# Kernel optimization log

Measured on AMD Instinct MI355X. Metric: run time of the kernel, lower is better.

The kernel has to match this reference:

```python
import jax, jax.numpy as jnp
import numpy as np

N_HEAD = 16
MA_K = 0.02          # sigmoid temperature in ma_k_activation
LEAKY_SLOPE = 0.02   # negative_slope in ma_q_activation
NEG_INF = -1e9


def setup_inputs() -> dict:
    key = jax.random.key(0)
    k1, k2, k3, k4 = jax.random.split(key, 4)
    B, T, C = 2, 2048, 1024
    x = jax.random.normal(k1, (B, T, C), dtype=jnp.float32)
    s = 1.0 / np.sqrt(C)
    W_attn = jax.random.normal(k2, (C, 2 * C), dtype=jnp.float32) * s
    W_k2 = jax.random.normal(k3, (C, C), dtype=jnp.float32) * s
    W_proj = jax.random.normal(k4, (C, C), dtype=jnp.float32) * s
    return {"x": x, "W_attn": W_attn, "W_k2": W_k2, "W_proj": W_proj}


def _heads(t, H):
    # [B,T,C] -> [B,H,T,d]
    B, T, C = t.shape
    return t.reshape(B, T, H, C // H).transpose(0, 2, 1, 3)


def reference(x, W_attn, W_k2, W_proj):
    B, T, C = x.shape
    H = N_HEAD
    d = C // H
    scale = 1.0 / jnp.sqrt(jnp.asarray(d, x.dtype))

    qk = x @ W_attn                      # [B,T,2C]
    q, k = jnp.split(qk, 2, axis=-1)
    q = _heads(q, H)                     # [B,H,T,d]
    k = _heads(k, H)
    v = _heads(x, H)                     # v = x

    # --- AR branch: causal softmax attention ---
    scores = jnp.einsum('bhtd,bhsd->bhts', q, k) * scale
    causal = jnp.tril(jnp.ones((T, T), dtype=bool))
    scores = jnp.where(causal, scores, NEG_INF)
    attn = jax.nn.softmax(scores, axis=-1)
    y = jnp.einsum('bhts,bhsd->bhtd', attn, v)   # [B,H,T,d]

    # --- MA branch: causal, softmax-free linear attention on residual ---
    e = v[:, :, 1:, :] - y[:, :, :-1, :]          # [B,H,T-1,d]
    k2 = _heads(x[:, :-1, :] @ W_k2, H)           # [B,H,T-1,d]
    q2 = q[:, :, 1:, :]                           # [B,H,T-1,d]

    qa = -jax.nn.leaky_relu(-q2 * scale, negative_slope=LEAKY_SLOPE)
    ka = jax.nn.sigmoid(MA_K * (k2 * scale))

    w = jnp.einsum('bhtd,bhsd->bhts', qa, ka)     # [B,H,T-1,T-1]
    w = jnp.tril(w)
    y2 = jnp.einsum('bhts,bhsd->bhtd', w, e)      # [B,H,T-1,d]
    y2 = jnp.concatenate([jnp.zeros_like(y2[:, :, :1, :]), y2], axis=2)  # pad front

    def merge(t):  # [B,H,T,d] -> [B,T,C]
        return t.transpose(0, 2, 1, 3).reshape(B, T, C)

    return merge(y) @ W_proj + merge(y2) @ W_proj
```

## Files before the change

kernel.cpp:

```cpp
#include <hip/hip_runtime.h>

typedef unsigned short u16;
typedef u16   u16x4  __attribute__((ext_vector_type(4)));
typedef u16   u16x8  __attribute__((ext_vector_type(8)));
typedef __bf16 bf16x8 __attribute__((ext_vector_type(8)));
typedef float  f32x4  __attribute__((ext_vector_type(4)));

__device__ __forceinline__ float bf2f(u16 v) {
    unsigned u = ((unsigned)v) << 16;
    return __builtin_bit_cast(float, u);
}
__device__ __forceinline__ u16 f2bf(float f) {
    unsigned u = __builtin_bit_cast(unsigned, f);
    u += 0x7fffu + ((u >> 16) & 1u);
    return (u16)(u >> 16);
}

__device__ __forceinline__ void async16(const u16* g, u16* l) {
    __builtin_amdgcn_global_load_lds(
        (const __attribute__((address_space(1))) unsigned int*)g,
        (__attribute__((address_space(3))) unsigned int*)l,
        16, 0, 0);
}

__device__ __forceinline__ size_t kimg_idx(int bh, int s, int d) {
    return ((size_t)(bh * 32 + (s >> 6)) * 4096) + (size_t)(((d >> 3) * 64 + (s & 63)) * 8) + (d & 7);
}
__device__ __forceinline__ size_t vimg_idx(int bh, int s, int d) {
    return ((size_t)(bh * 32 + (s >> 6)) * 4096) + (size_t)((((s & 63) >> 3) * 64 + d) * 8) + (s & 7);
}

__device__ __forceinline__ size_t g128_idx(int m, int k) {
    return ((size_t)((m >> 7) * 32 + (k >> 5)) * 4096)
         + (size_t)((((k >> 3) & 3) * 128 + (m & 127)) * 8 + (k & 7));
}
__device__ __forceinline__ size_t g64_idx(int m, int k) {
    return ((size_t)((m >> 6) * 32 + (k >> 5)) * 2048)
         + (size_t)((((k >> 3) & 3) * 64 + (m & 63)) * 8 + (k & 7));
}

__global__ __launch_bounds__(256)
void convert_pack(const float* __restrict__ in, u16* __restrict__ xb,
                  u16* __restrict__ xpack, u16* __restrict__ agimg) {
    int i = blockIdx.x * 256 + threadIdx.x;
    int c8 = i & 127, row = i >> 7;
    int s = row & 2047, b = row >> 11;
    float4 v0 = ((const float4*)in)[(size_t)i * 2];
    float4 v1 = ((const float4*)in)[(size_t)i * 2 + 1];
    u16x8 o;
    o[0] = f2bf(v0.x); o[1] = f2bf(v0.y); o[2] = f2bf(v0.z); o[3] = f2bf(v0.w);
    o[4] = f2bf(v1.x); o[5] = f2bf(v1.y); o[6] = f2bf(v1.z); o[7] = f2bf(v1.w);
    ((u16x8*)xb)[i] = o;
    int h = c8 >> 3, d0 = (c8 & 7) * 8;
    size_t base = vimg_idx(b * 16 + h, s, d0);
#pragma unroll
    for (int j = 0; j < 8; ++j) xpack[base + j * 8] = o[j];
    *(u16x8*)&agimg[g128_idx(row, c8 * 8)] = o;
}

__global__ __launch_bounds__(256)
void prep_weights(const float* __restrict__ Wa, const float* __restrict__ Wk,
                  const float* __restrict__ Wp, u16* __restrict__ bgimg,
                  u16* __restrict__ bpimg) {
    __shared__ u16 tile[64][65];
    const int bx = blockIdx.x;
    const float* in; u16* img; int Cd, c0, nbase;
    if (bx < 32)      { in = Wa; img = bgimg; Cd = 2048; c0 = bx * 64;        nbase = c0; }
    else if (bx < 48) { in = Wk; img = bgimg; Cd = 1024; c0 = (bx - 32) * 64; nbase = 2048 + c0; }
    else              { in = Wp; img = bpimg; Cd = 1024; c0 = (bx - 48) * 64; nbase = c0; }
    const int r0 = blockIdx.y * 64;
    const int tid = threadIdx.x;
#pragma unroll
    for (int i = 0; i < 16; ++i) {
        int idx = tid + i * 256;
        int r = idx >> 6, c = idx & 63;
        tile[r][c] = f2bf(in[(size_t)(r0 + r) * Cd + c0 + c]);
    }
    __syncthreads();
#pragma unroll
    for (int ii = 0; ii < 16; ++ii) {
        int u = tid + ii * 256;
        int s = u >> 11, kk = (u >> 9) & 3, nr = (u >> 3) & 63, e = u & 7;
        int r = s * 32 + kk * 8 + e;
        int n = nbase + nr, k = r0 + r;
        size_t o = (size_t)((n >> 7) * 32 + (k >> 5)) * 4096
                 + (size_t)(kk * 1024 + (n & 127) * 8 + e);
        img[o] = tile[r][nr];
    }
}

__global__ __launch_bounds__(256, 3)
void gemm_fused(const u16* __restrict__ Aimg, const u16* __restrict__ Bimg,
                u16* __restrict__ qs, u16* __restrict__ kpack,
                u16* __restrict__ kapack) {
    const int NT = 32;
    __shared__ __align__(16) u16 As[3][4][128][8];
    __shared__ __align__(16) u16 Bs[3][4][128][8];
    const int tid = threadIdx.x;
    const int wave = tid >> 6, lane = tid & 63;
    const int m0 = blockIdx.y * 128, n0 = blockIdx.x * 128;
    const int wm = (wave >> 1) * 64, wn = (wave & 1) * 64;
    const int q = lane >> 4, mr = lane & 15;

    const u16* gA = Aimg + (size_t)blockIdx.y * 32 * 4096;
    const u16* gB = Bimg + (size_t)blockIdx.x * 32 * 4096;
    u16* const lA = &As[0][0][0][0];
    u16* const lB = &Bs[0][0][0][0];
    const int d0 = tid * 8, d1 = (256 + tid) * 8;

    f32x4 acc[4][4];
#pragma unroll
    for (int i = 0; i < 4; ++i)
#pragma unroll
        for (int j = 0; j < 4; ++j) acc[i][j] = f32x4{0.f, 0.f, 0.f, 0.f};

    async16(gA + d0,        lA + d0);
    async16(gA + d1,        lA + d1);
    async16(gB + d0,        lB + d0);
    async16(gB + d1,        lB + d1);
    async16(gA + 4096 + d0, lA + 4096 + d0);
    async16(gA + 4096 + d1, lA + 4096 + d1);
    async16(gB + 4096 + d0, lB + 4096 + d0);
    async16(gB + 4096 + d1, lB + 4096 + d1);

    int co = 0;
    int io = 2 * 4096;
    for (int t = 0; t < NT; ++t) {
        if (t < NT - 1) asm volatile("s_waitcnt vmcnt(4)" ::: "memory");
        else            asm volatile("s_waitcnt vmcnt(0)" ::: "memory");
        __syncthreads();
        if (t + 2 < NT) {
            const int sg = (t + 2) * 4096;
            async16(gA + sg + d0, lA + io + d0);
            async16(gA + sg + d1, lA + io + d1);
            async16(gB + sg + d0, lB + io + d0);
            async16(gB + sg + d1, lB + io + d1);
        }
        bf16x8 af[4], bfr[4];
#pragma unroll
        for (int i = 0; i < 4; ++i)
            af[i]  = *(const bf16x8*)(lA + co + (size_t)(q * 128 + wm + i * 16 + mr) * 8);
#pragma unroll
        for (int j = 0; j < 4; ++j)
            bfr[j] = *(const bf16x8*)(lB + co + (size_t)(q * 128 + wn + j * 16 + mr) * 8);
#pragma unroll
        for (int i = 0; i < 4; ++i)
#pragma unroll
            for (int j = 0; j < 4; ++j)
                acc[i][j] = __builtin_amdgcn_mfma_f32_16x16x32_bf16(af[i], bfr[j], acc[i][j], 0, 0, 0);
        co += 4096; if (co == 3 * 4096) co = 0;
        io += 4096; if (io == 3 * 4096) io = 0;
    }
#pragma unroll
    for (int i = 0; i < 4; ++i)
#pragma unroll
        for (int j = 0; j < 4; ++j)
#pragma unroll
            for (int r = 0; r < 4; ++r) {
                int m = m0 + wm + i * 16 + q * 4 + r;
                int n = n0 + wn + j * 16 + mr;
                float v = acc[i][j][r];
                int b = m >> 11, s = m & 2047;
                if (n < 1024) {
                    qs[(size_t)m * 1024 + n] = f2bf(v * 0.125f);
                } else if (n < 2048) {
                    int nn = n - 1024;
                    kpack[kimg_idx(b * 16 + (nn >> 6), s, nn & 63)] = f2bf(v);
                } else {
                    int nn = n - 2048;
                    kapack[kimg_idx(b * 16 + (nn >> 6), s, nn & 63)] =
                        f2bf(1.f / (1.f + __expf(-0.0025f * v)));
                }
            }
}

__global__ __launch_bounds__(256, 2)
void gemm64(const u16* __restrict__ Aimg, const u16* __restrict__ Bimg,
            float* __restrict__ Cv, int N, int K) {
    const int NT = 32;
    __shared__ __align__(16) u16 As[3][4][64][8];
    __shared__ __align__(16) u16 Bs[3][4][128][8];
    const int tid = threadIdx.x;
    const int wave = tid >> 6, lane = tid & 63;
    const int m0 = blockIdx.y * 64, n0 = blockIdx.x * 128;
    const int wn0 = wave * 32;
    const int q = lane >> 4, mr = lane & 15;

    const u16* gA = Aimg + (size_t)blockIdx.y * 32 * 2048;
    const u16* gB = Bimg + (size_t)blockIdx.x * 32 * 4096;
    u16* const lA = &As[0][0][0][0];
    u16* const lB = &Bs[0][0][0][0];
    const int d0 = tid * 8, d1 = (256 + tid) * 8;

    f32x4 acc[4][2];
#pragma unroll
    for (int i = 0; i < 4; ++i)
#pragma unroll
        for (int j = 0; j < 2; ++j) acc[i][j] = f32x4{0.f, 0.f, 0.f, 0.f};

    async16(gA + d0,        lA + d0);
    async16(gB + d0,        lB + d0);
    async16(gB + d1,        lB + d1);
    async16(gA + 2048 + d0, lA + 2048 + d0);
    async16(gB + 4096 + d0, lB + 4096 + d0);
    async16(gB + 4096 + d1, lB + 4096 + d1);

    int coA = 0, coB = 0, ioA = 2 * 2048, ioB = 2 * 4096;
    for (int t = 0; t < NT; ++t) {
        if (t < NT - 1) asm volatile("s_waitcnt vmcnt(3)" ::: "memory");
        else            asm volatile("s_waitcnt vmcnt(0)" ::: "memory");
        __syncthreads();
        if (t + 2 < NT) {
            async16(gA + (t + 2) * 2048 + d0, lA + ioA + d0);
            async16(gB + (t + 2) * 4096 + d0, lB + ioB + d0);
            async16(gB + (t + 2) * 4096 + d1, lB + ioB + d1);
        }
        bf16x8 af[4], bfr[2];
#pragma unroll
        for (int i = 0; i < 4; ++i)
            af[i]  = *(const bf16x8*)(lA + coA + (size_t)(q * 64 + i * 16 + mr) * 8);
#pragma unroll
        for (int j = 0; j < 2; ++j)
            bfr[j] = *(const bf16x8*)(lB + coB + (size_t)(q * 128 + wn0 + j * 16 + mr) * 8);
#pragma unroll
        for (int i = 0; i < 4; ++i)
#pragma unroll
            for (int j = 0; j < 2; ++j)
                acc[i][j] = __builtin_amdgcn_mfma_f32_16x16x32_bf16(af[i], bfr[j], acc[i][j], 0, 0, 0);
        coA += 2048; if (coA == 3 * 2048) coA = 0;
        coB += 4096; if (coB == 3 * 4096) coB = 0;
        ioA += 2048; if (ioA == 3 * 2048) ioA = 0;
        ioB += 4096; if (ioB == 3 * 4096) ioB = 0;
    }
#pragma unroll
    for (int i = 0; i < 4; ++i)
#pragma unroll
        for (int j = 0; j < 2; ++j)
#pragma unroll
            for (int r = 0; r < 4; ++r) {
                int m = m0 + i * 16 + q * 4 + r;
                int n = n0 + wn0 + j * 16 + mr;
                Cv[(size_t)m * N + n] = acc[i][j][r];
            }
}

__global__ __launch_bounds__(256, 2)
void flash_mfma(const u16* __restrict__ qs, const u16* __restrict__ kpack,
                const u16* __restrict__ xpack, u16* __restrict__ Opart,
                float* __restrict__ lpart) {
    __shared__ __align__(16) u16 Ks[8][64][8];
    __shared__ __align__(16) u16 Vs[8][64][8];
    __shared__ __align__(16) u16 Ps[4][16][72];
    const int bh = blockIdx.y, b = bh >> 4, hc = (bh & 15) * 64;
    const int z = blockIdx.z;
    const int tid = threadIdx.x, w = tid >> 6, lane = tid & 63;
    const int n16 = lane & 15, quad = lane >> 4;
    const u16* kbase = kpack + (size_t)bh * 32 * 4096;
    const u16* vbase = xpack + (size_t)bh * 32 * 4096;
    u16* Ob = Opart + (size_t)z * 4096 * 1024;
    float* lb = lpart + z * 65536;

    for (int rep = 0; rep < 2; ++rep) {
        const int T = rep ? 15 - (int)blockIdx.x : (int)blockIdx.x;
        const int t0 = T * 128;
        const int nchunk = 2 * T + 2;

        bf16x8 qf[2][2];
#pragma unroll
        for (int mt = 0; mt < 2; ++mt) {
            const int trow = t0 + (w + mt * 4) * 16 + n16;
            const u16* qp = &qs[(size_t)(b * 2048 + trow) * 1024 + hc + quad * 8];
            qf[mt][0] = *(const bf16x8*)qp;
            qf[mt][1] = *(const bf16x8*)(qp + 32);
        }

        f32x4 O[2][4];
        float lsum[2][4];
#pragma unroll
        for (int mt = 0; mt < 2; ++mt)
#pragma unroll
            for (int jt = 0; jt < 4; ++jt) { O[mt][jt] = f32x4{0.f, 0.f, 0.f, 0.f}; }
#pragma unroll
        for (int mt = 0; mt < 2; ++mt)
#pragma unroll
            for (int r = 0; r < 4; ++r) lsum[mt][r] = 0.f;

        u16x8 kr0, kr1, vr0, vr1;
        auto pref = [&](int c) {
            const u16* kc = kbase + (size_t)c * 4096;
            const u16* vc = vbase + (size_t)c * 4096;
            kr0 = *(const u16x8*)(kc + tid * 8);
            kr1 = *(const u16x8*)(kc + (256 + tid) * 8);
            vr0 = *(const u16x8*)(vc + tid * 8);
            vr1 = *(const u16x8*)(vc + (256 + tid) * 8);
        };
        if (z < nchunk) pref(z);

        for (int c = z; c < nchunk; c += 2) {
            __syncthreads();
            *(u16x8*)((u16*)Ks + tid * 8)         = kr0;
            *(u16x8*)((u16*)Ks + (256 + tid) * 8) = kr1;
            *(u16x8*)((u16*)Vs + tid * 8)         = vr0;
            *(u16x8*)((u16*)Vs + (256 + tid) * 8) = vr1;
            __syncthreads();
            if (c + 2 < nchunk) pref(c + 2);

            f32x4 S[2][4];
#pragma unroll
            for (int mt = 0; mt < 2; ++mt)
#pragma unroll
                for (int jt = 0; jt < 4; ++jt) S[mt][jt] = f32x4{0.f, 0.f, 0.f, 0.f};
#pragma unroll
            for (int ks = 0; ks < 2; ++ks)
#pragma unroll
                for (int jt = 0; jt < 4; ++jt) {
                    bf16x8 kf = *(const bf16x8*)&Ks[ks * 4 + quad][jt * 16 + n16][0];
                    S[0][jt] = __builtin_amdgcn_mfma_f32_16x16x32_bf16(qf[0][ks], kf, S[0][jt], 0, 0, 0);
                    S[1][jt] = __builtin_amdgcn_mfma_f32_16x16x32_bf16(qf[1][ks], kf, S[1][jt], 0, 0, 0);
                }
            bf16x8 vf[2][4];
#pragma unroll
            for (int ks = 0; ks < 2; ++ks)
#pragma unroll
                for (int jt = 0; jt < 4; ++jt)
                    vf[ks][jt] = *(const bf16x8*)&Vs[ks * 4 + quad][jt * 16 + n16][0];

#pragma unroll
            for (int mt = 0; mt < 2; ++mt) {
                if (mt == 0 && c == 2 * T + 1) continue;
                float p[4][4];
#pragma unroll
                for (int reg = 0; reg < 4; ++reg)
#pragma unroll
                    for (int jt = 0; jt < 4; ++jt)
                        p[reg][jt] = __expf(S[mt][jt][reg]);
                if (c == 2 * T + mt) {
#pragma unroll
                    for (int reg = 0; reg < 4; ++reg) {
                        const int tr = t0 + (w + mt * 4) * 16 + quad * 4 + reg;
#pragma unroll
                        for (int jt = 0; jt < 4; ++jt)
                            if (c * 64 + jt * 16 + n16 > tr) p[reg][jt] = 0.f;
                    }
                }
#pragma unroll
                for (int reg = 0; reg < 4; ++reg) {
                    lsum[mt][reg] += (p[reg][0] + p[reg][1]) + (p[reg][2] + p[reg][3]);
#pragma unroll
                    for (int jt = 0; jt < 4; ++jt)
                        Ps[w][quad * 4 + reg][jt * 16 + n16] = f2bf(p[reg][jt]);
                }
                bf16x8 pf[2];
#pragma unroll
                for (int ks = 0; ks < 2; ++ks)
                    pf[ks] = *(const bf16x8*)&Ps[w][n16][ks * 32 + quad * 8];
#pragma unroll
                for (int ks = 0; ks < 2; ++ks)
#pragma unroll
                    for (int jt = 0; jt < 4; ++jt)
                        O[mt][jt] = __builtin_amdgcn_mfma_f32_16x16x32_bf16(pf[ks], vf[ks][jt], O[mt][jt], 0, 0, 0);
            }
        }

#pragma unroll
        for (int mt = 0; mt < 2; ++mt)
#pragma unroll
            for (int reg = 0; reg < 4; ++reg) {
                float l = lsum[mt][reg];
#pragma unroll
                for (int off = 1; off < 16; off <<= 1) l += __shfl_xor(l, off, 64);
                const int tr = t0 + (w + mt * 4) * 16 + quad * 4 + reg;
                if (n16 == 0) lb[bh * 2048 + tr] = l;
                const size_t row = (size_t)(b * 2048 + tr) * 1024 + hc;
#pragma unroll
                for (int jt = 0; jt < 4; ++jt)
                    Ob[row + jt * 16 + n16] = f2bf(O[mt][jt][reg]);
            }
    }
}

__global__ __launch_bounds__(256)
void combine_flash(const u16* __restrict__ Opart, const float* __restrict__ lpart,
                   const u16* __restrict__ xb, u16* __restrict__ y,
                   u16* __restrict__ epack) {
    int i = blockIdx.x * 256 + threadIdx.x;
    int c4 = i & 255, row = i >> 8, t = row & 2047, b = row >> 11;
    int h = c4 >> 4, d0 = (c4 & 15) * 4;
    size_t off = (size_t)row * 1024 + c4 * 4;
    u16x4 o0 = *(const u16x4*)&Opart[off];
    u16x4 o1 = *(const u16x4*)&Opart[(size_t)4096 * 1024 + off];
    int lrow = (b * 16 + h) * 2048 + t;
    float inv = 1.f / (lpart[lrow] + lpart[65536 + lrow]);
    float y0 = (bf2f(o0.x) + bf2f(o1.x)) * inv;
    float y1 = (bf2f(o0.y) + bf2f(o1.y)) * inv;
    float y2 = (bf2f(o0.z) + bf2f(o1.z)) * inv;
    float y3 = (bf2f(o0.w) + bf2f(o1.w)) * inv;
    u16x4 yo;
    yo.x = f2bf(y0); yo.y = f2bf(y1); yo.z = f2bf(y2); yo.w = f2bf(y3);
    *(u16x4*)&y[off] = yo;
    float e0 = 0.f, e1 = 0.f, e2 = 0.f, e3 = 0.f;
    if (t < 2047) {
        u16x4 xv = *(const u16x4*)&xb[off + 1024];
        e0 = bf2f(xv.x) - y0; e1 = bf2f(xv.y) - y1;
        e2 = bf2f(xv.z) - y2; e3 = bf2f(xv.w) - y3;
    }
    size_t base = vimg_idx(b * 16 + h, t, d0);
    epack[base]      = f2bf(e0);
    epack[base + 8]  = f2bf(e1);
    epack[base + 16] = f2bf(e2);
    epack[base + 24] = f2bf(e3);
}

__global__ __launch_bounds__(256, 2)
void arma_mfma(const u16* __restrict__ qs, const u16* __restrict__ kapack,
               const u16* __restrict__ epack, u16* __restrict__ Opart) {
    __shared__ __align__(16) u16 Ks[8][64][8];
    __shared__ __align__(16) u16 Es[8][64][8];
    __shared__ __align__(16) u16 Ps[4][16][72];
    const int bh = blockIdx.y, b = bh >> 4, hc = (bh & 15) * 64;
    const int z = blockIdx.z;
    const int tid = threadIdx.x, w = tid >> 6, lane = tid & 63;
    const int n16 = lane & 15, quad = lane >> 4;
    const u16* kbase = kapack + (size_t)bh * 32 * 4096;
    const u16* vbase = epack + (size_t)bh * 32 * 4096;
    u16* Ob = Opart + (size_t)z * 4096 * 1024;

    for (int rep = 0; rep < 2; ++rep) {
        const int T = rep ? 15 - (int)blockIdx.x : (int)blockIdx.x;
        const int t0 = T * 128;
        const int nchunk = 2 * T + 2;

        bf16x8 qf[2][2];
#pragma unroll
        for (int mt = 0; mt < 2; ++mt) {
            const int trow = t0 + (w + mt * 4) * 16 + n16;
            const u16* qp = &qs[(size_t)(b * 2048 + trow) * 1024 + hc + quad * 8];
#pragma unroll
            for (int ks = 0; ks < 2; ++ks) {
                u16x8 qv = *(const u16x8*)(qp + ks * 32);
                u16x8 o;
#pragma unroll
                for (int j = 0; j < 8; ++j) {
                    float zv = bf2f(qv[j]);
                    o[j] = f2bf(zv < 0.f ? zv : 0.02f * zv);
                }
                qf[mt][ks] = __builtin_bit_cast(bf16x8, o);
            }
        }

        f32x4 O[2][4];
#pragma unroll
        for (int mt = 0; mt < 2; ++mt)
#pragma unroll
            for (int jt = 0; jt < 4; ++jt) O[mt][jt] = f32x4{0.f, 0.f, 0.f, 0.f};

        u16x8 kr0, kr1, vr0, vr1;
        auto pref = [&](int c) {
            const u16* kc = kbase + (size_t)c * 4096;
            const u16* vc = vbase + (size_t)c * 4096;
            kr0 = *(const u16x8*)(kc + tid * 8);
            kr1 = *(const u16x8*)(kc + (256 + tid) * 8);
            vr0 = *(const u16x8*)(vc + tid * 8);
            vr1 = *(const u16x8*)(vc + (256 + tid) * 8);
        };
        if (z < nchunk) pref(z);

        for (int c = z; c < nchunk; c += 2) {
            __syncthreads();
            *(u16x8*)((u16*)Ks + tid * 8)         = kr0;
            *(u16x8*)((u16*)Ks + (256 + tid) * 8) = kr1;
            *(u16x8*)((u16*)Es + tid * 8)         = vr0;
            *(u16x8*)((u16*)Es + (256 + tid) * 8) = vr1;
            __syncthreads();
            if (c + 2 < nchunk) pref(c + 2);

            f32x4 S[2][4];
#pragma unroll
            for (int mt = 0; mt < 2; ++mt)
#pragma unroll
                for (int jt = 0; jt < 4; ++jt) S[mt][jt] = f32x4{0.f, 0.f, 0.f, 0.f};
#pragma unroll
            for (int ks = 0; ks < 2; ++ks)
#pragma unroll
                for (int jt = 0; jt < 4; ++jt) {
                    bf16x8 kf = *(const bf16x8*)&Ks[ks * 4 + quad][jt * 16 + n16][0];
                    S[0][jt] = __builtin_amdgcn_mfma_f32_16x16x32_bf16(qf[0][ks], kf, S[0][jt], 0, 0, 0);
                    S[1][jt] = __builtin_amdgcn_mfma_f32_16x16x32_bf16(qf[1][ks], kf, S[1][jt], 0, 0, 0);
                }
            bf16x8 vf[2][4];
#pragma unroll
            for (int ks = 0; ks < 2; ++ks)
#pragma unroll
                for (int jt = 0; jt < 4; ++jt)
                    vf[ks][jt] = *(const bf16x8*)&Es[ks * 4 + quad][jt * 16 + n16][0];

#pragma unroll
            for (int mt = 0; mt < 2; ++mt) {
                if (mt == 0 && c == 2 * T + 1) continue;
                if (c == 2 * T + mt) {
#pragma unroll
                    for (int reg = 0; reg < 4; ++reg) {
                        const int tr = t0 + (w + mt * 4) * 16 + quad * 4 + reg;
#pragma unroll
                        for (int jt = 0; jt < 4; ++jt)
                            if (c * 64 + jt * 16 + n16 >= tr) S[mt][jt][reg] = 0.f;
                    }
                }
#pragma unroll
                for (int reg = 0; reg < 4; ++reg)
#pragma unroll
                    for (int jt = 0; jt < 4; ++jt)
                        Ps[w][quad * 4 + reg][jt * 16 + n16] = f2bf(S[mt][jt][reg]);
                bf16x8 pf[2];
#pragma unroll
                for (int ks = 0; ks < 2; ++ks)
                    pf[ks] = *(const bf16x8*)&Ps[w][n16][ks * 32 + quad * 8];
#pragma unroll
                for (int ks = 0; ks < 2; ++ks)
#pragma unroll
                    for (int jt = 0; jt < 4; ++jt)
                        O[mt][jt] = __builtin_amdgcn_mfma_f32_16x16x32_bf16(pf[ks], vf[ks][jt], O[mt][jt], 0, 0, 0);
            }
        }

#pragma unroll
        for (int mt = 0; mt < 2; ++mt)
#pragma unroll
            for (int reg = 0; reg < 4; ++reg) {
                const int tr = t0 + (w + mt * 4) * 16 + quad * 4 + reg;
                const size_t row = (size_t)(b * 2048 + tr) * 1024 + hc;
#pragma unroll
                for (int jt = 0; jt < 4; ++jt)
                    Ob[row + jt * 16 + n16] = f2bf(O[mt][jt][reg]);
            }
    }
}

__global__ __launch_bounds__(256)
void combine_arma(const u16* __restrict__ Opart, const u16* __restrict__ y,
                  u16* __restrict__ ysimg) {
    int i = blockIdx.x * 256 + threadIdx.x;
    int c8 = i & 127, row = i >> 7;
    size_t off = (size_t)i * 8;
    u16x8 o0 = *(const u16x8*)&Opart[off];
    u16x8 o1 = *(const u16x8*)&Opart[(size_t)4096 * 1024 + off];
    u16x8 yv = *(const u16x8*)&y[off];
    u16x8 r;
#pragma unroll
    for (int j = 0; j < 8; ++j)
        r[j] = f2bf(bf2f(yv[j]) + bf2f(o0[j]) + bf2f(o1[j]));
    *(u16x8*)&ysimg[g64_idx(row, c8 * 8)] = r;
}

extern "C" void kernel_launch(void* const* d_in, const int* in_sizes, int n_in,
                              void* d_out, int out_size, void* d_ws, size_t ws_size,
                              hipStream_t stream) {
    const float* x      = (const float*)d_in[0];
    const float* W_attn = (const float*)d_in[1];
    const float* W_k2   = (const float*)d_in[2];
    const float* W_proj = (const float*)d_in[3];
    float* out = (float*)d_out;

    char* w = (char*)d_ws;
    u16* xb      = (u16*)w; w += (size_t)4096 * 1024 * 2;
    u16* bgimg   = (u16*)w; w += (size_t)3072 * 1024 * 2;
    u16* bpimg   = (u16*)w; w += (size_t)1024 * 1024 * 2;
    u16* qs      = (u16*)w; w += (size_t)4096 * 1024 * 2;
    u16* kpack   = (u16*)w; w += (size_t)4096 * 1024 * 2;
    u16* kapack  = (u16*)w; w += (size_t)4096 * 1024 * 2;
    u16* xpack   = (u16*)w; w += (size_t)4096 * 1024 * 2;
    u16* y       = (u16*)w; w += (size_t)4096 * 1024 * 2;
    u16* epack   = (u16*)w; w += (size_t)4096 * 1024 * 2;
    u16* Opart   = (u16*)w; w += (size_t)2 * 4096 * 1024 * 2;
    float* lpart = (float*)w; w += (size_t)2 * 65536 * 4;
    u16* agimg = Opart;
    u16* ysimg = xb;

    convert_pack<<<dim3(2048), dim3(256), 0, stream>>>(x, xb, xpack, agimg);
    prep_weights<<<dim3(64, 16), dim3(256), 0, stream>>>(W_attn, W_k2, W_proj,
                                                         bgimg, bpimg);
    gemm_fused<<<dim3(24, 32), dim3(256), 0, stream>>>(agimg, bgimg, qs, kpack, kapack);
    flash_mfma<<<dim3(8, 32, 2), dim3(256), 0, stream>>>(qs, kpack, xpack, Opart, lpart);
    combine_flash<<<dim3(4096), dim3(256), 0, stream>>>(Opart, lpart, xb, y, epack);
    arma_mfma<<<dim3(8, 32, 2), dim3(256), 0, stream>>>(qs, kapack, epack, Opart);
    combine_arma<<<dim3(2048), dim3(256), 0, stream>>>(Opart, y, ysimg);
    gemm64<<<dim3(8, 64), dim3(256), 0, stream>>>(ysimg, bpimg, out, 1024, 1024);
}
```

Baseline: 261.5 us.

## Load K/V fragments directly from global memory, dropping LDS staging and barriers

In both attention kernels, the cooperative copy of each K/V chunk into shared memory is removed, along with its two barriers per iteration. Each wave now loads its MFMA fragments straight from the packed global layout into registers. This cuts LDS traffic and synchronisation. In exchange, each chunk is read from global memory by all four waves (relying on cache), and the register prefetch of the next chunk is lost, which may expose load latency.

```diff
diff --git a/kernel.cpp b/kernel.cpp
--- a/kernel.cpp
+++ b/kernel.cpp
@@ -248,8 +248,6 @@
 void flash_mfma(const u16* __restrict__ qs, const u16* __restrict__ kpack,
                 const u16* __restrict__ xpack, u16* __restrict__ Opart,
                 float* __restrict__ lpart) {
-    __shared__ __align__(16) u16 Ks[8][64][8];
-    __shared__ __align__(16) u16 Vs[8][64][8];
     __shared__ __align__(16) u16 Ps[4][16][72];
     const int bh = blockIdx.y, b = bh >> 4, hc = (bh & 15) * 64;
     const int z = blockIdx.z;
@@ -260,6 +258,9 @@
     u16* Ob = Opart + (size_t)z * 4096 * 1024;
     float* lb = lpart + z * 65536;
 
+    const int fo0 = (quad * 64 + n16) * 8;
+    const int fo1 = ((4 + quad) * 64 + n16) * 8;
+
     for (int rep = 0; rep < 2; ++rep) {
         const int T = rep ? 15 - (int)blockIdx.x : (int)blockIdx.x;
         const int t0 = T * 128;
@@ -285,25 +286,17 @@
 #pragma unroll
             for (int r = 0; r < 4; ++r) lsum[mt][r] = 0.f;
 
-        u16x8 kr0, kr1, vr0, vr1;
-        auto pref = [&](int c) {
+        for (int c = z; c < nchunk; c += 2) {
             const u16* kc = kbase + (size_t)c * 4096;
             const u16* vc = vbase + (size_t)c * 4096;
-            kr0 = *(const u16x8*)(kc + tid * 8);
-            kr1 = *(const u16x8*)(kc + (256 + tid) * 8);
-            vr0 = *(const u16x8*)(vc + tid * 8);
-            vr1 = *(const u16x8*)(vc + (256 + tid) * 8);
-        };
-        if (z < nchunk) pref(z);
-
-        for (int c = z; c < nchunk; c += 2) {
-            __syncthreads();
-            *(u16x8*)((u16*)Ks + tid * 8)         = kr0;
-            *(u16x8*)((u16*)Ks + (256 + tid) * 8) = kr1;
-            *(u16x8*)((u16*)Vs + tid * 8)         = vr0;
-            *(u16x8*)((u16*)Vs + (256 + tid) * 8) = vr1;
-            __syncthreads();
-            if (c + 2 < nchunk) pref(c + 2);
+            bf16x8 kf[2][4], vf[2][4];
+#pragma unroll
+            for (int jt = 0; jt < 4; ++jt) {
+                kf[0][jt] = *(const bf16x8*)(kc + fo0 + jt * 128);
+                kf[1][jt] = *(const bf16x8*)(kc + fo1 + jt * 128);
+                vf[0][jt] = *(const bf16x8*)(vc + fo0 + jt * 128);
+                vf[1][jt] = *(const bf16x8*)(vc + fo1 + jt * 128);
+            }
 
             f32x4 S[2][4];
 #pragma unroll
@@ -314,16 +307,9 @@
             for (int ks = 0; ks < 2; ++ks)
 #pragma unroll
                 for (int jt = 0; jt < 4; ++jt) {
-                    bf16x8 kf = *(const bf16x8*)&Ks[ks * 4 + quad][jt * 16 + n16][0];
-                    S[0][jt] = __builtin_amdgcn_mfma_f32_16x16x32_bf16(qf[0][ks], kf, S[0][jt], 0, 0, 0);
-                    S[1][jt] = __builtin_amdgcn_mfma_f32_16x16x32_bf16(qf[1][ks], kf, S[1][jt], 0, 0, 0);
-                }
-            bf16x8 vf[2][4];
-#pragma unroll
-            for (int ks = 0; ks < 2; ++ks)
-#pragma unroll
-                for (int jt = 0; jt < 4; ++jt)
-                    vf[ks][jt] = *(const bf16x8*)&Vs[ks * 4 + quad][jt * 16 + n16][0];
+                    S[0][jt] = __builtin_amdgcn_mfma_f32_16x16x32_bf16(qf[0][ks], kf[ks][jt], S[0][jt], 0, 0, 0);
+                    S[1][jt] = __builtin_amdgcn_mfma_f32_16x16x32_bf16(qf[1][ks], kf[ks][jt], S[1][jt], 0, 0, 0);
+                }
 
 #pragma unroll
             for (int mt = 0; mt < 2; ++mt) {
@@ -414,8 +400,6 @@
 __global__ __launch_bounds__(256, 2)
 void arma_mfma(const u16* __restrict__ qs, const u16* __restrict__ kapack,
                const u16* __restrict__ epack, u16* __restrict__ Opart) {
-    __shared__ __align__(16) u16 Ks[8][64][8];
-    __shared__ __align__(16) u16 Es[8][64][8];
     __shared__ __align__(16) u16 Ps[4][16][72];
     const int bh = blockIdx.y, b = bh >> 4, hc = (bh & 15) * 64;
     const int z = blockIdx.z;
@@ -425,6 +409,9 @@
     const u16* vbase = epack + (size_t)bh * 32 * 4096;
     u16* Ob = Opart + (size_t)z * 4096 * 1024;
 
+    const int fo0 = (quad * 64 + n16) * 8;
+    const int fo1 = ((4 + quad) * 64 + n16) * 8;
+
     for (int rep = 0; rep < 2; ++rep) {
         const int T = rep ? 15 - (int)blockIdx.x : (int)blockIdx.x;
         const int t0 = T * 128;
@@ -454,25 +441,17 @@
 #pragma unroll
             for (int jt = 0; jt < 4; ++jt) O[mt][jt] = f32x4{0.f, 0.f, 0.f, 0.f};
 
-        u16x8 kr0, kr1, vr0, vr1;
-        auto pref = [&](int c) {
+        for (int c = z; c < nchunk; c += 2) {
             const u16* kc = kbase + (size_t)c * 4096;
             const u16* vc = vbase + (size_t)c * 4096;
-            kr0 = *(const u16x8*)(kc + tid * 8);
-            kr1 = *(const u16x8*)(kc + (256 + tid) * 8);
-            vr0 = *(const u16x8*)(vc + tid * 8);
-            vr1 = *(const u16x8*)(vc + (256 + tid) * 8);
-        };
-        if (z < nchunk) pref(z);
-
-        for (int c = z; c < nchunk; c += 2) {
-            __syncthreads();
-            *(u16x8*)((u16*)Ks + tid * 8)         = kr0;
-            *(u16x8*)((u16*)Ks + (256 + tid) * 8) = kr1;
-            *(u16x8*)((u16*)Es + tid * 8)         = vr0;
-            *(u16x8*)((u16*)Es + (256 + tid) * 8) = vr1;
-            __syncthreads();
-            if (c + 2 < nchunk) pref(c + 2);
+            bf16x8 kf[2][4], vf[2][4];
+#pragma unroll
+            for (int jt = 0; jt < 4; ++jt) {
+                kf[0][jt] = *(const bf16x8*)(kc + fo0 + jt * 128);
+                kf[1][jt] = *(const bf16x8*)(kc + fo1 + jt * 128);
+                vf[0][jt] = *(const bf16x8*)(vc + fo0 + jt * 128);
+                vf[1][jt] = *(const bf16x8*)(vc + fo1 + jt * 128);
+            }
 
             f32x4 S[2][4];
 #pragma unroll
@@ -483,16 +462,9 @@
             for (int ks = 0; ks < 2; ++ks)
 #pragma unroll
                 for (int jt = 0; jt < 4; ++jt) {
-                    bf16x8 kf = *(const bf16x8*)&Ks[ks * 4 + quad][jt * 16 + n16][0];
-                    S[0][jt] = __builtin_amdgcn_mfma_f32_16x16x32_bf16(qf[0][ks], kf, S[0][jt], 0, 0, 0);
-                    S[1][jt] = __builtin_amdgcn_mfma_f32_16x16x32_bf16(qf[1][ks], kf, S[1][jt], 0, 0, 0);
-                }
-            bf16x8 vf[2][4];
-#pragma unroll
-            for (int ks = 0; ks < 2; ++ks)
-#pragma unroll
-                for (int jt = 0; jt < 4; ++jt)
-                    vf[ks][jt] = *(const bf16x8*)&Es[ks * 4 + quad][jt * 16 + n16][0];
+                    S[0][jt] = __builtin_amdgcn_mfma_f32_16x16x32_bf16(qf[0][ks], kf[ks][jt], S[0][jt], 0, 0, 0);
+                    S[1][jt] = __builtin_amdgcn_mfma_f32_16x16x32_bf16(qf[1][ks], kf[ks][jt], S[1][jt], 0, 0, 0);
+                }
 
 #pragma unroll
             for (int mt = 0; mt < 2; ++mt) {
```

Result: slower. 271.7 us (+3.9%).
